# Optimization experiments

Hardware: AMD Instinct MI355X
Metric: run time of the kernel (lower is better)

## Reference

```python
import jax, jax.numpy as jnp
import numpy as np

P, Q, R, H1, H2, PH, B = 32, 32, 8, 128, 64, 16, 8192
PAIRS = P * Q
OUT = PAIRS * R  # X_Z_layer output units


def _pairwise_mask(p, q, r):
    # rows i*q+k correspond to pair (x_i, z_k): connected to x_i and z_k only
    mx = np.zeros((p * q, p), np.float32)
    for i in range(p):
        mx[i * q:(i + 1) * q, i] = 1.0
    mz = np.tile(np.eye(q, dtype=np.float32), (p, 1))
    m = np.concatenate([mx, mz], axis=1)          # [p*q, p+q]
    return np.repeat(m, r, axis=0)                 # [p*q*r, p+q]


def setup_inputs() -> dict:
    key = jax.random.key(0)
    ks = jax.random.split(key, 24)
    rn = lambda k, s, sc=0.1: jax.random.normal(k, s, jnp.float32) * sc
    x = jax.random.normal(ks[0], (B, P), jnp.float32)
    z = jax.random.normal(ks[1], (B, Q), jnp.float32)
    # X_mlp: P -> H1 -> H2 -> 1
    xw1, xb1 = rn(ks[2], (P, H1)), rn(ks[3], (H1,))
    xw2, xb2 = rn(ks[4], (H1, H2)), rn(ks[5], (H2,))
    xw3, xb3 = rn(ks[6], (H2, 1)), rn(ks[7], (1,))
    # Z_mlp: Q -> H1 -> H2 -> 1
    zw1, zb1 = rn(ks[8], (Q, H1)), rn(ks[9], (H1,))
    zw2, zb2 = rn(ks[10], (Q if False else H1, H2)), rn(ks[11], (H2,))
    zw3, zb3 = rn(ks[12], (H2, 1)), rn(ks[13], (1,))
    # masked X_Z_layer: weight pre-multiplied by structured mask (as in __init__)
    mask = jnp.asarray(_pairwise_mask(P, Q, R))    # [OUT, P+Q]
    xzw = (rn(ks[14], (OUT, P + Q)) * mask).T      # [P+Q, OUT]
    xzb = rn(ks[15], (OUT,))
    # 1024 tiny per-pair MLPs: R -> PH (bias) -> 1 (no bias), stacked
    pw1 = rn(ks[16], (PAIRS, R, PH))
    pb1 = rn(ks[17], (PAIRS, PH))
    pw2 = rn(ks[18], (PAIRS, PH))
    return dict(x=x, z=z, xw1=xw1, xb1=xb1, xw2=xw2, xb2=xb2, xw3=xw3, xb3=xb3,
                zw1=zw1, zb1=zb1, zw2=zw2, zb2=zb2, zw3=zw3, zb3=zb3,
                xzw=xzw, xzb=xzb, pw1=pw1, pb1=pb1, pw2=pw2)


def reference(x, z, xw1, xb1, xw2, xb2, xw3, xb3,
              zw1, zb1, zw2, zb2, zw3, zb3, xzw, xzb, pw1, pb1, pw2):
    relu = jax.nn.relu
    # main-effect MLPs
    hx = relu(relu(x @ xw1 + xb1) @ xw2 + xb2)
    out_x = hx @ xw3 + xb3                         # [B,1]
    hz = relu(relu(z @ zw1 + zb1) @ zw2 + zb2)
    out_z = hz @ zw3 + zb3                         # [B,1]
    # masked interaction layer
    xz = jnp.concatenate([x, z], axis=1)           # [B, P+Q]
    h = relu(xz @ xzw + xzb)                       # [B, OUT]
    # all 1024 per-pair MLPs as one batched GEMM
    hp = h.reshape(h.shape[0], PAIRS, R)           # [B, pairs, R]
    t = relu(jnp.einsum('bpr,prh->bph', hp, pw1) + pb1)
    out_xz = jnp.einsum('bph,ph->b', t, pw2)[:, None]  # sum over pairs -> [B,1]
    return out_x + out_z + out_xz
```

## Files before the change

### kernel.cpp

```cpp
#include <hip/hip_runtime.h>

#define B_TOT 8192
#define PP 32
#define QQ 32
#define RR 8
#define H1 128
#define H2 64
#define PHH 16
#define PAIRS 1024
#define OUT_UNITS 8192

#define NBLK_MM 256
#define NBLK_IA 2048

typedef float f32x16 __attribute__((ext_vector_type(16)));
typedef short s16x8  __attribute__((ext_vector_type(8)));

union FragU { s16x8 v; unsigned int u[4]; };

__device__ inline unsigned int pack_bf16(float lo, float hi) {
    unsigned int r;
    asm("v_cvt_pk_bf16_f32 %0, %1, %2" : "=v"(r) : "v"(lo), "v"(hi));
    return r;
}

union SharedU {
    union {
        struct {
            float zT[16][256];
            float4 lwx[16][2];
            float4 lwz[16][2];
            float4 lhb[16][2];
            unsigned lpw1T[17][16][4];
            float lpb[16][16];
            float lpw2[16][16];
        } s;
        float red[256][33];
    } ia;
    struct {
        union {
            float xT[32][68];
            float h1T[128][68];
        };
    } mm;
};

__global__ __launch_bounds__(512, 6) void fused_k(
    const float* __restrict__ x, const float* __restrict__ z,
    const float* __restrict__ xw1, const float* __restrict__ xb1,
    const float* __restrict__ xw2, const float* __restrict__ xb2,
    const float* __restrict__ xw3, const float* __restrict__ xb3,
    const float* __restrict__ zw1, const float* __restrict__ zb1,
    const float* __restrict__ zw2, const float* __restrict__ zb2,
    const float* __restrict__ zw3, const float* __restrict__ zb3,
    const float* __restrict__ xzw, const float* __restrict__ xzb,
    const float* __restrict__ pw1, const float* __restrict__ pb1,
    const float* __restrict__ pw2, float* __restrict__ out)
{
    __shared__ SharedU sh;
    const int bid  = blockIdx.x;
    const int t    = threadIdx.x;
    const int w    = t >> 6;
    const int lane = t & 63;

    if (bid >= NBLK_MM) {
        const int ib    = bid - NBLK_MM;
        const int bx    = ib & 31;
        const int y     = ib >> 5;
        const int m     = lane & 31;
        const int kh    = lane >> 5;
        const int jj    = m & 15;
        const int cph   = m >> 4;
        const int b0    = bx * 256;
        const int i_x   = y >> 1;
        const int k0    = (y & 1) * 16;
        const int pair0 = y * 16;

        {
            int row = t >> 1;
            int c8  = (t & 1) * 8;
            const float* src = z + (size_t)(b0 + row) * 32 + k0 + c8;
            float4 a4 = *reinterpret_cast<const float4*>(src);
            float4 b4 = *reinterpret_cast<const float4*>(src + 4);
            sh.ia.s.zT[c8+0][row] = a4.x; sh.ia.s.zT[c8+1][row] = a4.y;
            sh.ia.s.zT[c8+2][row] = a4.z; sh.ia.s.zT[c8+3][row] = a4.w;
            sh.ia.s.zT[c8+4][row] = b4.x; sh.ia.s.zT[c8+5][row] = b4.y;
            sh.ia.s.zT[c8+6][row] = b4.z; sh.ia.s.zT[c8+7][row] = b4.w;
        }
        if (t < 128) {
            int p = t >> 3, c = t & 7;
            int gp = pair0 + p;
            reinterpret_cast<float*>(sh.ia.s.lwx)[t] = xzw[(size_t)i_x * OUT_UNITS + gp*8 + c];
            reinterpret_cast<float*>(sh.ia.s.lwz)[t] = xzw[(size_t)(32 + k0 + p) * OUT_UNITS + gp*8 + c];
            reinterpret_cast<float*>(sh.ia.s.lhb)[t] = xzb[gp*8 + c];
        }
        if (t < 256) {
            int p = t >> 4, j = t & 15;
            int gp = pair0 + p;
            sh.ia.s.lpb[p][j]  = pb1[gp*PHH + j];
            sh.ia.s.lpw2[p][j] = pw2[gp*PHH + j];
        }
        #pragma unroll
        for (int it = 0; it < 2; ++it) {
            int idx = t + it * 512;
            int p = idx >> 6, u = (idx >> 4) & 3, j = idx & 15;
            int gp = pair0 + p;
            float lo = pw1[(size_t)gp * 128 + (2*u)*16 + j];
            float hi = pw1[(size_t)gp * 128 + (2*u+1)*16 + j];
            sh.ia.s.lpw1T[p][j][u] = pack_bf16(lo, hi);
        }
        if (t < 64) reinterpret_cast<unsigned*>(sh.ia.s.lpw1T[16])[t] = 0u;

        const int bl = w * 32 + m;
        const float xv = x[(size_t)(b0 + bl) * 32 + i_x];
        __syncthreads();

        f32x16 acc;
        #pragma unroll
        for (int r = 0; r < 16; ++r) acc[r] = 0.f;

        const bool realB = (kh == cph);

        #pragma unroll 2
        for (int ppl = 0; ppl < 8; ++ppl) {
            const int pAl = 2*ppl + kh;
            const int pBl = 2*ppl + cph;

            const float zv = sh.ia.s.zT[pAl][bl];
            const float4 wxa = sh.ia.s.lwx[pAl][0], wxb = sh.ia.s.lwx[pAl][1];
            const float4 wza = sh.ia.s.lwz[pAl][0], wzb = sh.ia.s.lwz[pAl][1];
            const float4 hba = sh.ia.s.lhb[pAl][0], hbb = sh.ia.s.lhb[pAl][1];

            float h0[8];
            h0[0] = fmaxf(fmaf(xv, wxa.x, fmaf(zv, wza.x, hba.x)), 0.f);
            h0[1] = fmaxf(fmaf(xv, wxa.y, fmaf(zv, wza.y, hba.y)), 0.f);
            h0[2] = fmaxf(fmaf(xv, wxa.z, fmaf(zv, wza.z, hba.z)), 0.f);
            h0[3] = fmaxf(fmaf(xv, wxa.w, fmaf(zv, wza.w, hba.w)), 0.f);
            h0[4] = fmaxf(fmaf(xv, wxb.x, fmaf(zv, wzb.x, hbb.x)), 0.f);
            h0[5] = fmaxf(fmaf(xv, wxb.y, fmaf(zv, wzb.y, hbb.y)), 0.f);
            h0[6] = fmaxf(fmaf(xv, wxb.z, fmaf(zv, wzb.z, hbb.z)), 0.f);
            h0[7] = fmaxf(fmaf(xv, wxb.w, fmaf(zv, wzb.w, hbb.w)), 0.f);

            FragU a0, bf;
            a0.u[0] = pack_bf16(h0[0], h0[1]);
            a0.u[1] = pack_bf16(h0[2], h0[3]);
            a0.u[2] = pack_bf16(h0[4], h0[5]);
            a0.u[3] = pack_bf16(h0[6], h0[7]);

            const unsigned* bq = sh.ia.s.lpw1T[realB ? pBl : 16][jj];
            bf.u[0] = bq[0]; bf.u[1] = bq[1]; bf.u[2] = bq[2]; bf.u[3] = bq[3];

            const float pbv = sh.ia.s.lpb[pBl][jj];
            const float w2v = sh.ia.s.lpw2[pBl][jj];

            f32x16 cpb;
            #pragma unroll
            for (int r = 0; r < 16; ++r) cpb[r] = pbv;

            f32x16 d = __builtin_amdgcn_mfma_f32_32x32x16_bf16(a0.v, bf.v, cpb, 0, 0, 0);

            #pragma unroll
            for (int r = 0; r < 16; ++r)
                acc[r] = fmaf(fmaxf(d[r], 0.f), w2v, acc[r]);
        }

        __syncthreads();
        #pragma unroll
        for (int r = 0; r < 16; ++r) {
            int rowf = (r & 3) + 8 * (r >> 2) + 4 * kh;
            sh.ia.red[w * 32 + rowf][m] = acc[r];
        }
        __syncthreads();
        if (t < 256) {
            float s = 0.f;
            #pragma unroll
            for (int c = 0; c < 32; ++c) s += sh.ia.red[t][c];
            atomicAdd(out + b0 + t, s);
        }
    } else {
        const int btile = bid & 127;
        const int which = bid >> 7;
        const float* in = which ? z   : x;
        const float* w1 = which ? zw1 : xw1;
        const float* b1 = which ? zb1 : xb1;
        const float* w2 = which ? zw2 : xw2;
        const float* b2 = which ? zb2 : xb2;
        const float* w3 = which ? zw3 : xw3;
        const float* b3 = which ? zb3 : xb3;
        const int b0 = btile * 64;
        const int bw = w * 8;

        {
            int row = t >> 3;
            int c4  = (t & 7) * 4;
            float4 v = *reinterpret_cast<const float4*>(in + (size_t)(b0 + row) * 32 + c4);
            sh.mm.xT[c4+0][row] = v.x; sh.mm.xT[c4+1][row] = v.y;
            sh.mm.xT[c4+2][row] = v.z; sh.mm.xT[c4+3][row] = v.w;
        }
        __syncthreads();

        const int j1 = lane, j2 = lane + 64;
        float a1[8], a2[8];
        {
            float bb1 = b1[j1], bb2 = b1[j2];
            #pragma unroll
            for (int i = 0; i < 8; ++i) { a1[i] = bb1; a2[i] = bb2; }
        }
        #pragma unroll 4
        for (int m = 0; m < 32; ++m) {
            const float4* xr = reinterpret_cast<const float4*>(&sh.mm.xT[m][bw]);
            float4 xa = xr[0], xb = xr[1];
            float wv1 = w1[m*H1 + j1];
            float wv2 = w1[m*H1 + j2];
            a1[0] = fmaf(xa.x, wv1, a1[0]); a2[0] = fmaf(xa.x, wv2, a2[0]);
            a1[1] = fmaf(xa.y, wv1, a1[1]); a2[1] = fmaf(xa.y, wv2, a2[1]);
            a1[2] = fmaf(xa.z, wv1, a1[2]); a2[2] = fmaf(xa.z, wv2, a2[2]);
            a1[3] = fmaf(xa.w, wv1, a1[3]); a2[3] = fmaf(xa.w, wv2, a2[3]);
            a1[4] = fmaf(xb.x, wv1, a1[4]); a2[4] = fmaf(xb.x, wv2, a2[4]);
            a1[5] = fmaf(xb.y, wv1, a1[5]); a2[5] = fmaf(xb.y, wv2, a2[5]);
            a1[6] = fmaf(xb.z, wv1, a1[6]); a2[6] = fmaf(xb.z, wv2, a2[6]);
            a1[7] = fmaf(xb.w, wv1, a1[7]); a2[7] = fmaf(xb.w, wv2, a2[7]);
        }
        __syncthreads();
        #pragma unroll
        for (int i = 0; i < 8; ++i) {
            sh.mm.h1T[j1][bw + i] = fmaxf(a1[i], 0.f);
            sh.mm.h1T[j2][bw + i] = fmaxf(a2[i], 0.f);
        }
        __syncthreads();

        float hacc[8];
        {
            float b2v = b2[lane];
            #pragma unroll
            for (int i = 0; i < 8; ++i) hacc[i] = b2v;
        }
        #pragma unroll 4
        for (int m = 0; m < 128; ++m) {
            float w2v = w2[m*H2 + lane];
            const float4* hr = reinterpret_cast<const float4*>(&sh.mm.h1T[m][bw]);
            float4 ha = hr[0], hb = hr[1];
            hacc[0] = fmaf(ha.x, w2v, hacc[0]);
            hacc[1] = fmaf(ha.y, w2v, hacc[1]);
            hacc[2] = fmaf(ha.z, w2v, hacc[2]);
            hacc[3] = fmaf(ha.w, w2v, hacc[3]);
            hacc[4] = fmaf(hb.x, w2v, hacc[4]);
            hacc[5] = fmaf(hb.y, w2v, hacc[5]);
            hacc[6] = fmaf(hb.z, w2v, hacc[6]);
            hacc[7] = fmaf(hb.w, w2v, hacc[7]);
        }
        {
            float w3v = w3[lane];
            #pragma unroll
            for (int i = 0; i < 8; ++i) hacc[i] = fmaxf(hacc[i], 0.f) * w3v;
        }
        __syncthreads();
        #pragma unroll
        for (int i = 0; i < 8; ++i)
            sh.mm.h1T[bw + i][lane] = hacc[i];
        __syncthreads();
        if (t < 64) {
            float s = b3[0];
            const float4* rr = reinterpret_cast<const float4*>(&sh.mm.h1T[t][0]);
            #pragma unroll
            for (int c = 0; c < 16; ++c) {
                float4 v = rr[c];
                s += (v.x + v.y) + (v.z + v.w);
            }
            atomicAdd(out + b0 + t, s);
        }
    }
}

extern "C" void kernel_launch(void* const* d_in, const int* in_sizes, int n_in,
                              void* d_out, int out_size, void* d_ws, size_t ws_size,
                              hipStream_t stream) {
    const float* x   = (const float*)d_in[0];
    const float* z   = (const float*)d_in[1];
    const float* xw1 = (const float*)d_in[2];
    const float* xb1 = (const float*)d_in[3];
    const float* xw2 = (const float*)d_in[4];
    const float* xb2 = (const float*)d_in[5];
    const float* xw3 = (const float*)d_in[6];
    const float* xb3 = (const float*)d_in[7];
    const float* zw1 = (const float*)d_in[8];
    const float* zb1 = (const float*)d_in[9];
    const float* zw2 = (const float*)d_in[10];
    const float* zb2 = (const float*)d_in[11];
    const float* zw3 = (const float*)d_in[12];
    const float* zb3 = (const float*)d_in[13];
    const float* xzw = (const float*)d_in[14];
    const float* xzb = (const float*)d_in[15];
    const float* pw1 = (const float*)d_in[16];
    const float* pb1 = (const float*)d_in[17];
    const float* pw2 = (const float*)d_in[18];
    float* out = (float*)d_out;

    hipMemsetAsync(out, 0, (size_t)out_size * sizeof(float), stream);

    fused_k<<<dim3(NBLK_MM + NBLK_IA), 512, 0, stream>>>(
        x, z, xw1, xb1, xw2, xb2, xw3, xb3,
        zw1, zb1, zw2, zb2, zw3, zb3,
        xzw, xzb, pw1, pb1, pw2, out);
}
```

Before: 118.7 us.

## Process two x-rows per interaction block to halve block count and atomics

Each interaction block now handles two pair-groups that share the same z slice (x rows i_xb and i_xb+1), so the z transpose and zv loads are reused across both. The interaction grid shrinks from 2048 to 1024 blocks, halving the number of atomicAdd reductions to the output. Pair bias and second-layer weights are interleaved into one float2 array to merge two LDS loads. The final reduction is split across all 512 threads with a shuffle. Shared memory per block grows, which may reduce occupancy, and there is less block-level parallelism.

```diff
diff --git a/kernel.cpp b/kernel.cpp
--- a/kernel.cpp
+++ b/kernel.cpp
@@ -11,7 +11,7 @@
 #define OUT_UNITS 8192
 
 #define NBLK_MM 256
-#define NBLK_IA 2048
+#define NBLK_IA 1024
 
 typedef float f32x16 __attribute__((ext_vector_type(16)));
 typedef short s16x8  __attribute__((ext_vector_type(8)));
@@ -28,12 +28,11 @@
     union {
         struct {
             float zT[16][256];
-            float4 lwx[16][2];
-            float4 lwz[16][2];
-            float4 lhb[16][2];
-            unsigned lpw1T[17][16][4];
-            float lpb[16][16];
-            float lpw2[16][16];
+            float4 lwx[32][2];
+            float4 lwz[32][2];
+            float4 lhb[32][2];
+            unsigned lpw1T[33][16][4];
+            float lpbw[32][16][2];
         } s;
         float red[256][33];
     } ia;
@@ -66,15 +65,19 @@
     if (bid >= NBLK_MM) {
         const int ib    = bid - NBLK_MM;
         const int bx    = ib & 31;
-        const int y     = ib >> 5;
+        const int y2    = ib >> 5;
         const int m     = lane & 31;
         const int kh    = lane >> 5;
         const int jj    = m & 15;
         const int cph   = m >> 4;
         const int b0    = bx * 256;
-        const int i_x   = y >> 1;
-        const int k0    = (y & 1) * 16;
-        const int pair0 = y * 16;
+        const int par   = y2 & 1;
+        const int i_xb  = y2 & ~1;
+        const int k0    = par * 16;
+        const int oy0   = 2 * i_xb + par;
+        const int oy1   = oy0 + 2;
+        const int pair0_0 = oy0 * 16;
+        const int pair0_1 = oy1 * 16;
 
         {
             int row = t >> 1;
@@ -87,32 +90,38 @@
             sh.ia.s.zT[c8+4][row] = b4.x; sh.ia.s.zT[c8+5][row] = b4.y;
             sh.ia.s.zT[c8+6][row] = b4.z; sh.ia.s.zT[c8+7][row] = b4.w;
         }
-        if (t < 128) {
-            int p = t >> 3, c = t & 7;
-            int gp = pair0 + p;
-            reinterpret_cast<float*>(sh.ia.s.lwx)[t] = xzw[(size_t)i_x * OUT_UNITS + gp*8 + c];
-            reinterpret_cast<float*>(sh.ia.s.lwz)[t] = xzw[(size_t)(32 + k0 + p) * OUT_UNITS + gp*8 + c];
-            reinterpret_cast<float*>(sh.ia.s.lhb)[t] = xzb[gp*8 + c];
-        }
         if (t < 256) {
+            int sb  = t >> 7;
+            int idx = t & 127;
+            int p = idx >> 3, c = idx & 7;
+            int gp = (sb ? pair0_1 : pair0_0) + p;
+            int pl = sb * 16 + p;
+            reinterpret_cast<float*>(sh.ia.s.lwx)[pl*8 + c] = xzw[(size_t)(i_xb + sb) * OUT_UNITS + gp*8 + c];
+            reinterpret_cast<float*>(sh.ia.s.lwz)[pl*8 + c] = xzw[(size_t)(32 + k0 + p) * OUT_UNITS + gp*8 + c];
+            reinterpret_cast<float*>(sh.ia.s.lhb)[pl*8 + c] = xzb[gp*8 + c];
+        }
+        {
             int p = t >> 4, j = t & 15;
-            int gp = pair0 + p;
-            sh.ia.s.lpb[p][j]  = pb1[gp*PHH + j];
-            sh.ia.s.lpw2[p][j] = pw2[gp*PHH + j];
-        }
-        #pragma unroll
-        for (int it = 0; it < 2; ++it) {
+            int gp = ((p >> 4) ? pair0_1 : pair0_0) + (p & 15);
+            float2 bw;
+            bw.x = pb1[gp*PHH + j];
+            bw.y = pw2[gp*PHH + j];
+            *reinterpret_cast<float2*>(sh.ia.s.lpbw[p][j]) = bw;
+        }
+        #pragma unroll
+        for (int it = 0; it < 4; ++it) {
             int idx = t + it * 512;
             int p = idx >> 6, u = (idx >> 4) & 3, j = idx & 15;
-            int gp = pair0 + p;
+            int gp = ((p >> 4) ? pair0_1 : pair0_0) + (p & 15);
             float lo = pw1[(size_t)gp * 128 + (2*u)*16 + j];
             float hi = pw1[(size_t)gp * 128 + (2*u+1)*16 + j];
             sh.ia.s.lpw1T[p][j][u] = pack_bf16(lo, hi);
         }
-        if (t < 64) reinterpret_cast<unsigned*>(sh.ia.s.lpw1T[16])[t] = 0u;
+        if (t < 64) reinterpret_cast<unsigned*>(sh.ia.s.lpw1T[32])[t] = 0u;
 
         const int bl = w * 32 + m;
-        const float xv = x[(size_t)(b0 + bl) * 32 + i_x];
+        const float2 xv2 = *reinterpret_cast<const float2*>(
+            x + (size_t)(b0 + bl) * 32 + i_xb);
         __syncthreads();
 
         f32x16 acc;
@@ -123,45 +132,51 @@
 
         #pragma unroll 2
         for (int ppl = 0; ppl < 8; ++ppl) {
-            const int pAl = 2*ppl + kh;
-            const int pBl = 2*ppl + cph;
-
-            const float zv = sh.ia.s.zT[pAl][bl];
-            const float4 wxa = sh.ia.s.lwx[pAl][0], wxb = sh.ia.s.lwx[pAl][1];
-            const float4 wza = sh.ia.s.lwz[pAl][0], wzb = sh.ia.s.lwz[pAl][1];
-            const float4 hba = sh.ia.s.lhb[pAl][0], hbb = sh.ia.s.lhb[pAl][1];
-
-            float h0[8];
-            h0[0] = fmaxf(fmaf(xv, wxa.x, fmaf(zv, wza.x, hba.x)), 0.f);
-            h0[1] = fmaxf(fmaf(xv, wxa.y, fmaf(zv, wza.y, hba.y)), 0.f);
-            h0[2] = fmaxf(fmaf(xv, wxa.z, fmaf(zv, wza.z, hba.z)), 0.f);
-            h0[3] = fmaxf(fmaf(xv, wxa.w, fmaf(zv, wza.w, hba.w)), 0.f);
-            h0[4] = fmaxf(fmaf(xv, wxb.x, fmaf(zv, wzb.x, hbb.x)), 0.f);
-            h0[5] = fmaxf(fmaf(xv, wxb.y, fmaf(zv, wzb.y, hbb.y)), 0.f);
-            h0[6] = fmaxf(fmaf(xv, wxb.z, fmaf(zv, wzb.z, hbb.z)), 0.f);
-            h0[7] = fmaxf(fmaf(xv, wxb.w, fmaf(zv, wzb.w, hbb.w)), 0.f);
-
-            FragU a0, bf;
-            a0.u[0] = pack_bf16(h0[0], h0[1]);
-            a0.u[1] = pack_bf16(h0[2], h0[3]);
-            a0.u[2] = pack_bf16(h0[4], h0[5]);
-            a0.u[3] = pack_bf16(h0[6], h0[7]);
-
-            const unsigned* bq = sh.ia.s.lpw1T[realB ? pBl : 16][jj];
-            bf.u[0] = bq[0]; bf.u[1] = bq[1]; bf.u[2] = bq[2]; bf.u[3] = bq[3];
-
-            const float pbv = sh.ia.s.lpb[pBl][jj];
-            const float w2v = sh.ia.s.lpw2[pBl][jj];
-
-            f32x16 cpb;
-            #pragma unroll
-            for (int r = 0; r < 16; ++r) cpb[r] = pbv;
-
-            f32x16 d = __builtin_amdgcn_mfma_f32_32x32x16_bf16(a0.v, bf.v, cpb, 0, 0, 0);
-
-            #pragma unroll
-            for (int r = 0; r < 16; ++r)
-                acc[r] = fmaf(fmaxf(d[r], 0.f), w2v, acc[r]);
+            const int kA = 2*ppl + kh;
+            const int kB = 2*ppl + cph;
+            const float zv = sh.ia.s.zT[kA][bl];
+
+            #pragma unroll
+            for (int sb = 0; sb < 2; ++sb) {
+                const int pAl = sb*16 + kA;
+                const int pBl = sb*16 + kB;
+                const float xv = sb ? xv2.y : xv2.x;
+
+                const float4 wxa = sh.ia.s.lwx[pAl][0], wxb = sh.ia.s.lwx[pAl][1];
+                const float4 wza = sh.ia.s.lwz[pAl][0], wzb = sh.ia.s.lwz[pAl][1];
+                const float4 hba = sh.ia.s.lhb[pAl][0], hbb = sh.ia.s.lhb[pAl][1];
+
+                float h0[8];
+                h0[0] = fmaxf(fmaf(xv, wxa.x, fmaf(zv, wza.x, hba.x)), 0.f);
+                h0[1] = fmaxf(fmaf(xv, wxa.y, fmaf(zv, wza.y, hba.y)), 0.f);
+                h0[2] = fmaxf(fmaf(xv, wxa.z, fmaf(zv, wza.z, hba.z)), 0.f);
+                h0[3] = fmaxf(fmaf(xv, wxa.w, fmaf(zv, wza.w, hba.w)), 0.f);
+                h0[4] = fmaxf(fmaf(xv, wxb.x, fmaf(zv, wzb.x, hbb.x)), 0.f);
+                h0[5] = fmaxf(fmaf(xv, wxb.y, fmaf(zv, wzb.y, hbb.y)), 0.f);
+                h0[6] = fmaxf(fmaf(xv, wxb.z, fmaf(zv, wzb.z, hbb.z)), 0.f);
+                h0[7] = fmaxf(fmaf(xv, wxb.w, fmaf(zv, wzb.w, hbb.w)), 0.f);
+
+                FragU a0, bf;
+                a0.u[0] = pack_bf16(h0[0], h0[1]);
+                a0.u[1] = pack_bf16(h0[2], h0[3]);
+                a0.u[2] = pack_bf16(h0[4], h0[5]);
+                a0.u[3] = pack_bf16(h0[6], h0[7]);
+
+                const unsigned* bq = sh.ia.s.lpw1T[realB ? pBl : 32][jj];
+                bf.u[0] = bq[0]; bf.u[1] = bq[1]; bf.u[2] = bq[2]; bf.u[3] = bq[3];
+
+                const float2 bw = *reinterpret_cast<const float2*>(sh.ia.s.lpbw[pBl][jj]);
+
+                f32x16 cpb;
+                #pragma unroll
+                for (int r = 0; r < 16; ++r) cpb[r] = bw.x;
+
+                f32x16 d = __builtin_amdgcn_mfma_f32_32x32x16_bf16(a0.v, bf.v, cpb, 0, 0, 0);
+
+                #pragma unroll
+                for (int r = 0; r < 16; ++r)
+                    acc[r] = fmaf(fmaxf(d[r], 0.f), bw.y, acc[r]);
+            }
         }
 
         __syncthreads();
@@ -171,11 +186,14 @@
             sh.ia.red[w * 32 + rowf][m] = acc[r];
         }
         __syncthreads();
-        if (t < 256) {
-            float s = 0.f;
-            #pragma unroll
-            for (int c = 0; c < 32; ++c) s += sh.ia.red[t][c];
-            atomicAdd(out + b0 + t, s);
+        {
+            int row = t >> 1, hh = t & 1;
+            const float* rr = &sh.ia.red[row][hh * 16];
+            float ssum = 0.f;
+            #pragma unroll
+            for (int c = 0; c < 16; ++c) ssum += rr[c];
+            ssum += __shfl_xor(ssum, 1);
+            if (hh == 0) atomicAdd(out + b0 + row, ssum);
         }
     } else {
         const int btile = bid & 127;
```

Measured after the change: 117.3 us. No clear change (-1.1%).
